# Optimization experiments

Hardware: AMD Instinct MI355X
Metric: run time of the kernel (lower is better)

Reference implementation:

```python
import jax, jax.numpy as jnp
import numpy as np

N, E, F_IN, EDGE_DIM, H, C, NUM_RELS = 20000, 160000, 64, 8, 4, 128, 4


def setup_inputs() -> dict:
    key = jax.random.key(0)
    ks = jax.random.split(key, 20)
    def rn(k, shape, s=0.05):
        return jax.random.normal(k, shape, jnp.float32) * s
    return {
        "x": rn(ks[0], (N, F_IN), 1.0),
        "edge_index": jax.random.randint(ks[1], (2, E), 0, N, dtype=jnp.int32),
        "edge_features": rn(ks[2], (E, EDGE_DIM), 1.0),
        "W1": rn(ks[3], (F_IN, H * C)), "a_src1": rn(ks[4], (H, C)), "a_dst1": rn(ks[5], (H, C)),
        "We1": rn(ks[6], (EDGE_DIM, H * C)), "a_e1": rn(ks[7], (H, C)), "b1": jnp.zeros((H * C,), jnp.float32),
        "W2": rn(ks[8], (H * C, H * C)), "a_src2": rn(ks[9], (H, C)), "a_dst2": rn(ks[10], (H, C)),
        "We2": rn(ks[11], (EDGE_DIM, H * C)), "a_e2": rn(ks[12], (H, C)), "b2": jnp.zeros((H * C,), jnp.float32),
        "Wd1": rn(ks[13], (2 * H * C, 256)), "bd1": jnp.zeros((256,), jnp.float32),
        "Wd2": rn(ks[14], (256, NUM_RELS)), "bd2": jnp.zeros((NUM_RELS,), jnp.float32),
    }


def _add_self_loops(ei, ea, n):
    # PyG add_self_loops with fill_value='mean': self-loop edge_attr is the
    # mean of incoming edge_attr per destination node (0 if no incoming edges).
    dst = ei[1]
    s = jax.ops.segment_sum(ea, dst, num_segments=n)
    cnt = jax.ops.segment_sum(jnp.ones((ea.shape[0], 1), ea.dtype), dst, num_segments=n)
    mean = s / jnp.maximum(cnt, 1.0)
    loop = jnp.arange(n, dtype=ei.dtype)
    ei2 = jnp.concatenate([ei, jnp.stack([loop, loop])], axis=1)
    ea2 = jnp.concatenate([ea, mean], axis=0)
    return ei2, ea2


def _gat_conv(x, ei, ea, W, a_s, a_d, We, a_e, b, n):
    ei, ea = _add_self_loops(ei, ea, n)
    src, dst = ei[0], ei[1]
    xp = (x @ W).reshape(n, H, C)                      # [N,H,C]
    alpha_s = jnp.einsum('nhc,hc->nh', xp, a_s)        # [N,H]
    alpha_d = jnp.einsum('nhc,hc->nh', xp, a_d)        # [N,H]
    ep = (ea @ We).reshape(-1, H, C)                   # [E',H,C]
    alpha_e = jnp.einsum('ehc,hc->eh', ep, a_e)        # [E',H]
    alpha = alpha_s[src] + alpha_d[dst] + alpha_e
    alpha = jax.nn.leaky_relu(alpha, 0.2)
    # segment softmax over edges sharing a destination node
    m = jax.ops.segment_max(alpha, dst, num_segments=n)
    ex = jnp.exp(alpha - m[dst])
    den = jax.ops.segment_sum(ex, dst, num_segments=n)
    w = ex / den[dst]                                   # [E',H]
    out = jax.ops.segment_sum(xp[src] * w[..., None], dst, num_segments=n)  # [N,H,C]
    return out.reshape(n, H * C) + b


def reference(x, edge_index, edge_features, W1, a_src1, a_dst1, We1, a_e1, b1,
              W2, a_src2, a_dst2, We2, a_e2, b2, Wd1, bd1, Wd2, bd2):
    n = x.shape[0]
    z = jax.nn.elu(_gat_conv(x, edge_index, edge_features, W1, a_src1, a_dst1, We1, a_e1, b1, n))
    z = jax.nn.elu(_gat_conv(z, edge_index, edge_features, W2, a_src2, a_dst2, We2, a_e2, b2, n))
    src, dst = edge_index[0], edge_index[1]
    rel = jnp.concatenate([z[src], z[dst]], axis=1)     # [E, 2*512]
    h = rel @ Wd1 + bd1                                 # dropout is identity at inference
    return jax.nn.sigmoid(h @ Wd2 + bd2)
```

## Files before the change

kernel.cpp:

```cpp
#include <hip/hip_runtime.h>
#include <hip/hip_bf16.h>
#include <math.h>

#define N_NODES 20000
#define N_EDGES 160000
#define FIN 64
#define EDGE_DIM 8
#define H_HEADS 4
#define C_CH 128
#define HC 512
#define NUM_RELS 4
#define E_TOT (N_EDGES + N_NODES)
#define E_PAD 320256

typedef __bf16 bf16x8 __attribute__((ext_vector_type(8)));
typedef __bf16 bf16x4 __attribute__((ext_vector_type(4)));
typedef float f32x4 __attribute__((ext_vector_type(4)));
typedef unsigned short u16x8 __attribute__((ext_vector_type(8)));

#define NZ4 ((N_NODES + E_PAD) / 4)
#define NM4 (E_PAD / 4)
__global__ void k_fill(int4* __restrict__ zbase, int4* __restrict__ mbase) {
    int tid = blockIdx.x * 256 + threadIdx.x;
    if (tid < NZ4) {
        zbase[tid] = make_int4(0, 0, 0, 0);
    } else if (tid < NZ4 + NM4) {
        mbase[tid - NZ4] = make_int4(-1, -1, -1, -1);
    }
}

#define NX4 (N_NODES * FIN / 4)
#define XB  (NX4 / 256)
#define W1B 8
#define W2B 64
#define PREPB 19
__global__ void k_prep_all(const float* __restrict__ x, __bf16* __restrict__ xb,
                           const float* __restrict__ W1, __bf16* __restrict__ Wt1,
                           const float* __restrict__ W2, __bf16* __restrict__ Wt2,
                           const float* __restrict__ We1, const float* __restrict__ ae1,
                           const float* __restrict__ We2, const float* __restrict__ ae2,
                           float* __restrict__ q1, float* __restrict__ q2,
                           const float* __restrict__ Wd1, const float* __restrict__ Wd2,
                           const float* __restrict__ bd1, const float* __restrict__ bd2,
                           float* __restrict__ M, float* __restrict__ cvec,
                           const float* __restrict__ as1, const float* __restrict__ ad1,
                           float* __restrict__ w1as, float* __restrict__ w1ad) {
    __shared__ float tile[64][65];
    int bid = blockIdx.x;
    int t = threadIdx.x;
    if (bid < XB) {
        int tid = bid * 256 + t;
        float4 v = *(const float4*)(x + (size_t)tid * 4);
        __bf16 o[4] = {(__bf16)v.x, (__bf16)v.y, (__bf16)v.z, (__bf16)v.w};
        *(ushort2*)(xb + (size_t)tid * 4) = *(ushort2*)o;
        *(ushort2*)(xb + (size_t)tid * 4 + 2) = *(ushort2*)(o + 2);
        return;
    }
    if (bid < XB + W1B) {
        int tn = bid - XB;
        int rr = t >> 6, cc = t & 63;
        #pragma unroll
        for (int i = 0; i < 16; ++i) {
            int row = rr * 16 + i;
            tile[row][cc] = W1[(size_t)row * HC + tn * 64 + cc];
        }
        __syncthreads();
        #pragma unroll
        for (int i = 0; i < 16; ++i) {
            int row = rr * 16 + i;
            Wt1[(size_t)(tn * 64 + row) * 64 + cc] = (__bf16)tile[cc][row];
        }
        return;
    }
    if (bid < XB + W1B + W2B) {
        int p2 = bid - XB - W1B;
        int tk = p2 >> 3, tn = p2 & 7;
        int rr = t >> 6, cc = t & 63;
        #pragma unroll
        for (int i = 0; i < 16; ++i) {
            int row = rr * 16 + i;
            tile[row][cc] = W2[(size_t)(tk * 64 + row) * HC + tn * 64 + cc];
        }
        __syncthreads();
        #pragma unroll
        for (int i = 0; i < 16; ++i) {
            int row = rr * 16 + i;
            Wt2[(size_t)(tn * 64 + row) * HC + tk * 64 + cc] = (__bf16)tile[cc][row];
        }
        return;
    }
    int pb = bid - XB - W1B - W2B;
    if (pb == 16) {
        if (t >= 64) return;
        const float* We = (t < 32) ? We1 : We2;
        const float* ae = (t < 32) ? ae1 : ae2;
        float* q = (t < 32) ? q1 : q2;
        int i = t & 31, h = i >> 3, d = i & 7;
        float s = 0.f;
        for (int c = 0; c < 128; ++c) s += We[d * 512 + h * 128 + c] * ae[h * 128 + c];
        q[i] = s;
    } else if (pb == 17 || pb == 18) {
        int h = t >> 6, k = t & 63;
        const float* av = (pb == 17) ? as1 : ad1;
        float* outp = (pb == 17) ? w1as : w1ad;
        float s = 0.f;
        for (int c = 0; c < 128; ++c) s += W1[(size_t)k * HC + h * 128 + c] * av[h * 128 + c];
        outp[h * 64 + k] = s;
    } else {
        int tid = pb * 256 + t;
        int i = tid >> 2, r = tid & 3;
        float s = 0.f;
        for (int k = 0; k < 256; ++k) s += Wd1[i * 256 + k] * Wd2[k * 4 + r];
        M[tid] = s;
        if (tid < 4) {
            float c = 0.f;
            for (int k = 0; k < 256; ++k) c += bd1[k] * Wd2[k * 4 + tid];
            cvec[tid] = c + bd2[tid];
        }
    }
}

#define LDP 40
__global__ __launch_bounds__(256)
void k_gemm_bf16(const __bf16* __restrict__ A, const __bf16* __restrict__ Bt,
                 __bf16* __restrict__ Ch, int M, int K,
                 const float* __restrict__ a_s2, const float* __restrict__ a_d2,
                 float* __restrict__ as_, float* __restrict__ ad_) {
    __shared__ __bf16 As[128 * LDP];
    __shared__ __bf16 Bs[128 * LDP];

    int nwg = gridDim.x;
    int f = blockIdx.x;
    int q = nwg >> 3, r = nwg & 7;
    int xcd = f & 7, idx = f >> 3;
    int wg = (xcd < r ? xcd * (q + 1) : r * (q + 1) + (xcd - r) * q) + idx;
    int by = wg >> 2, bx = wg & 3;
    int br = by * 128, bc = bx * 128;

    const int t = threadIdx.x;
    const int lane = t & 63;
    const int wid = t >> 6;
    const int wr = wid >> 1, wc = wid & 1;
    const int l15 = lane & 15, lkg = lane >> 4;

    const int srow = t >> 1, shalf = (t & 1) * 16;
    const int agr = br + srow;
    const __bf16* Ap = A + (size_t)agr * K + shalf;
    const __bf16* Bp = Bt + (size_t)(bc + srow) * K + shalf;

    f32x4 acc[4][4] = {};

    for (int k0 = 0; k0 < K; k0 += 32) {
        u16x8 av0 = {}, av1 = {};
        if (agr < M) {
            av0 = *(const u16x8*)(Ap + k0);
            av1 = *(const u16x8*)(Ap + k0 + 8);
        }
        u16x8 bv0 = *(const u16x8*)(Bp + k0);
        u16x8 bv1 = *(const u16x8*)(Bp + k0 + 8);
        *(u16x8*)(As + srow * LDP + shalf) = av0;
        *(u16x8*)(As + srow * LDP + shalf + 8) = av1;
        *(u16x8*)(Bs + srow * LDP + shalf) = bv0;
        *(u16x8*)(Bs + srow * LDP + shalf + 8) = bv1;
        __syncthreads();

        bf16x8 a[4], b[4];
        #pragma unroll
        for (int m = 0; m < 4; ++m)
            a[m] = *(const bf16x8*)(As + (wr * 64 + m * 16 + l15) * LDP + lkg * 8);
        #pragma unroll
        for (int n = 0; n < 4; ++n)
            b[n] = *(const bf16x8*)(Bs + (wc * 64 + n * 16 + l15) * LDP + lkg * 8);
        #pragma unroll
        for (int m = 0; m < 4; ++m)
            #pragma unroll
            for (int n = 0; n < 4; ++n)
                acc[m][n] = __builtin_amdgcn_mfma_f32_16x16x32_bf16(a[m], b[n], acc[m][n], 0, 0, 0);
        __syncthreads();
    }

    #pragma unroll
    for (int m = 0; m < 4; ++m) {
        int rbase = br + wr * 64 + m * 16 + lkg * 4;
        #pragma unroll
        for (int n = 0; n < 4; ++n) {
            int lcol = wc * 64 + n * 16 + l15;
            #pragma unroll
            for (int rg = 0; rg < 4; ++rg) {
                int gr = rbase + rg;
                if (gr < M)
                    Ch[((size_t)bx * N_NODES + gr) * 128 + lcol] = (__bf16)acc[m][n][rg];
            }
        }
    }

    float as_w[4], ad_w[4];
    #pragma unroll
    for (int n = 0; n < 4; ++n) {
        int col = wc * 64 + n * 16 + l15;
        as_w[n] = a_s2[bx * 128 + col];
        ad_w[n] = a_d2[bx * 128 + col];
    }
    float* sred = (float*)As;
    #pragma unroll
    for (int m = 0; m < 4; ++m) {
        #pragma unroll
        for (int rg = 0; rg < 4; ++rg) {
            float s = 0.f, d = 0.f;
            #pragma unroll
            for (int n = 0; n < 4; ++n) {
                float c = acc[m][n][rg];
                s += c * as_w[n];
                d += c * ad_w[n];
            }
            #pragma unroll
            for (int off = 1; off <= 8; off <<= 1) {
                s += __shfl_xor(s, off);
                d += __shfl_xor(d, off);
            }
            if (l15 == 0) {
                int lrow = wr * 64 + m * 16 + lkg * 4 + rg;
                sred[lrow * 2 + wc] = s;
                sred[256 + lrow * 2 + wc] = d;
            }
        }
    }
    __syncthreads();
    if (t < 128) {
        int gr = br + t;
        if (gr < M) {
            as_[gr * 4 + bx] = sred[t * 2] + sred[t * 2 + 1];
            ad_[gr * 4 + bx] = sred[256 + t * 2] + sred[256 + t * 2 + 1];
        }
    }
}

__global__ __launch_bounds__(256)
void k_gemm_head(const __bf16* __restrict__ aggb, const __bf16* __restrict__ Wt1,
                 const float* __restrict__ b1, __bf16* __restrict__ z1b, int M) {
    __shared__ __bf16 As[128 * LDP];
    __shared__ __bf16 Bs[128 * LDP];
    const int h = blockIdx.x;
    const int br = blockIdx.y * 128;

    const int t = threadIdx.x;
    const int lane = t & 63;
    const int wid = t >> 6;
    const int wr = wid >> 1, wc = wid & 1;
    const int l15 = lane & 15, lkg = lane >> 4;

    const int srow = t >> 1, shalf = (t & 1) * 16;
    const int agr = br + srow;
    const __bf16* Ap = aggb + (size_t)agr * 256 + h * 64 + shalf;
    const __bf16* Bp = Wt1 + (size_t)(h * 128 + srow) * 64 + shalf;

    f32x4 acc[4][4] = {};

    #pragma unroll
    for (int k0 = 0; k0 < 64; k0 += 32) {
        u16x8 av0 = {}, av1 = {};
        if (agr < M) {
            av0 = *(const u16x8*)(Ap + k0);
            av1 = *(const u16x8*)(Ap + k0 + 8);
        }
        u16x8 bv0 = *(const u16x8*)(Bp + k0);
        u16x8 bv1 = *(const u16x8*)(Bp + k0 + 8);
        *(u16x8*)(As + srow * LDP + shalf) = av0;
        *(u16x8*)(As + srow * LDP + shalf + 8) = av1;
        *(u16x8*)(Bs + srow * LDP + shalf) = bv0;
        *(u16x8*)(Bs + srow * LDP + shalf + 8) = bv1;
        __syncthreads();

        bf16x8 a[4], b[4];
        #pragma unroll
        for (int m = 0; m < 4; ++m)
            a[m] = *(const bf16x8*)(As + (wr * 64 + m * 16 + l15) * LDP + lkg * 8);
        #pragma unroll
        for (int n = 0; n < 4; ++n)
            b[n] = *(const bf16x8*)(Bs + (wc * 64 + n * 16 + l15) * LDP + lkg * 8);
        #pragma unroll
        for (int m = 0; m < 4; ++m)
            #pragma unroll
            for (int n = 0; n < 4; ++n)
                acc[m][n] = __builtin_amdgcn_mfma_f32_16x16x32_bf16(a[m], b[n], acc[m][n], 0, 0, 0);
        __syncthreads();
    }

    #pragma unroll
    for (int m = 0; m < 4; ++m) {
        int rbase = br + wr * 64 + m * 16 + lkg * 4;
        #pragma unroll
        for (int n = 0; n < 4; ++n) {
            int gcol = h * 128 + wc * 64 + n * 16 + l15;
            float bias = b1[gcol];
            #pragma unroll
            for (int rg = 0; rg < 4; ++rg) {
                int gr = rbase + rg;
                if (gr < M) {
                    float v = acc[m][n][rg] + bias;
                    v = (v > 0.f) ? v : expm1f(v);
                    z1b[(size_t)gr * HC + gcol] = (__bf16)v;
                }
            }
        }
    }
}

__global__ void k_count(const int* __restrict__ ei, int* __restrict__ counts) {
    int e = blockIdx.x * 256 + threadIdx.x;
    if (e >= E_TOT) return;
    int dst = (e < N_EDGES) ? ei[N_EDGES + e] : (e - N_EDGES);
    atomicAdd(counts + dst, 1);
}

__global__ __launch_bounds__(1024)
void k_scan(const int* __restrict__ counts, int* __restrict__ row_start,
            int* __restrict__ nxt) {
    __shared__ int part[1024];
    int t = threadIdx.x;
    int base = t * 20;
    int pre[20];
    int s = 0;
    #pragma unroll
    for (int i = 0; i < 20; ++i) {
        int idx = base + i;
        int c = (idx < N_NODES) ? ((counts[idx] + 7) & ~7) : 0;
        pre[i] = s; s += c;
    }
    part[t] = s;
    __syncthreads();
    for (int off = 1; off < 1024; off <<= 1) {
        int v = (t >= off) ? part[t - off] : 0;
        __syncthreads();
        part[t] += v;
        __syncthreads();
    }
    int excl = (t == 0) ? 0 : part[t - 1];
    #pragma unroll
    for (int i = 0; i < 20; ++i) {
        int idx = base + i;
        if (idx < N_NODES) { int v = excl + pre[i]; row_start[idx] = v; nxt[idx] = v; }
    }
    if (t == 1023) row_start[N_NODES] = part[1023];
}

__global__ void k_scatter(const int* __restrict__ ei, int* __restrict__ nxt,
                          int* __restrict__ csr_src, int* __restrict__ csr_eid,
                          int* __restrict__ csr_dst) {
    int e = blockIdx.x * 256 + threadIdx.x;
    if (e >= E_TOT) return;
    int src, dst;
    if (e < N_EDGES) { src = ei[e]; dst = ei[N_EDGES + e]; }
    else             { src = dst = e - N_EDGES; }
    int pos = atomicAdd(nxt + dst, 1);
    csr_src[pos] = src;
    csr_eid[pos] = e;
    csr_dst[pos] = dst;
}

__global__ void k_mean_csr(const int* __restrict__ row_start, const int* __restrict__ csr_eid,
                           const float* __restrict__ ef, float* __restrict__ meanf) {
    int n = blockIdx.x * 32 + (threadIdx.x >> 3);
    int d = threadIdx.x & 7;
    if (n >= N_NODES) return;
    int rs = row_start[n], re = row_start[n + 1];
    float s = 0.f; int c = 0;
    for (int i = rs; i < re; ++i) {
        unsigned eid = (unsigned)csr_eid[i];
        if (eid < N_EDGES) { s += ef[(size_t)eid * 8 + d]; ++c; }
    }
    meanf[n * 8 + d] = s / fmaxf((float)c, 1.f);
}

__global__ __launch_bounds__(256)
void k_nodeab(const __bf16* __restrict__ xb, const float* __restrict__ w1as,
              const float* __restrict__ w1ad, float* __restrict__ as_,
              float* __restrict__ ad_) {
    int n = blockIdx.x * 4 + (threadIdx.x >> 6);
    int lane = threadIdx.x & 63;
    if (n >= N_NODES) return;
    float xv = (float)xb[(size_t)n * 64 + lane];
    float s[4], d[4];
    #pragma unroll
    for (int h = 0; h < 4; ++h) {
        s[h] = xv * w1as[h * 64 + lane];
        d[h] = xv * w1ad[h * 64 + lane];
    }
    #pragma unroll
    for (int off = 32; off; off >>= 1) {
        #pragma unroll
        for (int h = 0; h < 4; ++h) {
            s[h] += __shfl_xor(s[h], off);
            d[h] += __shfl_xor(d[h], off);
        }
    }
    if (lane == 0) {
        *(float4*)(as_ + n * 4) = make_float4(s[0], s[1], s[2], s[3]);
        *(float4*)(ad_ + n * 4) = make_float4(d[0], d[1], d[2], d[3]);
    }
}

__global__ void k_edge_ex(const int* __restrict__ csr_src, const int* __restrict__ csr_dst,
                          const int* __restrict__ csr_eid, const float* __restrict__ ef,
                          const float* __restrict__ meanf, const float* __restrict__ q,
                          const float* __restrict__ as_, const float* __restrict__ ad_,
                          float* __restrict__ wbuf) {
    int i = blockIdx.x * 256 + threadIdx.x;
    if (i >= E_PAD) return;
    int eid = csr_eid[i];
    if (eid == -1) {
        *(float4*)(wbuf + (size_t)i * 4) = make_float4(0.f, 0.f, 0.f, 0.f);
        return;
    }
    int src = csr_src[i], dst = csr_dst[i];
    const float* fe = (eid < N_EDGES) ? (ef + (size_t)eid * 8)
                                      : (meanf + (size_t)(eid - N_EDGES) * 8);
    float f[8];
    #pragma unroll
    for (int d = 0; d < 8; ++d) f[d] = fe[d];
    float4 asv = *(const float4*)(as_ + src * 4);
    float4 adv = *(const float4*)(ad_ + dst * 4);
    const float* asp = &asv.x;
    const float* adp = &adv.x;
    float4 o;
    float* op = &o.x;
    #pragma unroll
    for (int h = 0; h < 4; ++h) {
        float ae = 0.f;
        #pragma unroll
        for (int d = 0; d < 8; ++d) ae += f[d] * q[h * 8 + d];
        float a = asp[h] + adp[h] + ae;
        a = (a > 0.f) ? a : 0.2f * a;
        op[h] = expf(a);
    }
    *(float4*)(wbuf + (size_t)i * 4) = o;
}

__global__ __launch_bounds__(256)
void k_gather1(const int* __restrict__ row_start, const int* __restrict__ csr_src,
               const float* __restrict__ wbuf, const __bf16* __restrict__ xb,
               __bf16* __restrict__ aggb) {
    int wv = threadIdx.x >> 6;
    int n = blockIdx.x * 4 + wv;
    int lane = threadIdx.x & 63;
    if (n >= N_NODES) return;
    int rs = row_start[n], re = row_start[n + 1];
    float acc[4] = {};
    float den[4] = {};

    for (int i = rs; i < re; i += 8) {
        unsigned short xr[8];
        float4 wr[8];
        #pragma unroll
        for (int p = 0; p < 8; ++p) {
            int sp = csr_src[i + p];
            xr[p] = *(const unsigned short*)(xb + (size_t)sp * 64 + lane);
            wr[p] = *(const float4*)(wbuf + (size_t)(i + p) * 4);
        }
        __builtin_amdgcn_sched_barrier(0);
        #pragma unroll
        for (int p = 0; p < 8; ++p) {
            float xv = (float)*(const __bf16*)&xr[p];
            acc[0] += wr[p].x * xv; den[0] += wr[p].x;
            acc[1] += wr[p].y * xv; den[1] += wr[p].y;
            acc[2] += wr[p].z * xv; den[2] += wr[p].z;
            acc[3] += wr[p].w * xv; den[3] += wr[p].w;
        }
    }
    #pragma unroll
    for (int h = 0; h < 4; ++h)
        aggb[(size_t)n * 256 + h * 64 + lane] = (__bf16)(acc[h] / den[h]);
}

__global__ __launch_bounds__(256)
void k_gather2h(const int* __restrict__ row_start, const int* __restrict__ csr_src,
                const float* __restrict__ wbuf, const __bf16* __restrict__ xph,
                const float* __restrict__ b2, const float* __restrict__ Mm,
                float* __restrict__ Up, float* __restrict__ Vp) {
    int h = blockIdx.y;
    int wv = threadIdx.x >> 6;
    int n = blockIdx.x * 4 + wv;
    int lane = threadIdx.x & 63;
    if (n >= N_NODES) return;
    int rs = row_start[n], re = row_start[n + 1];
    const __bf16* xbase = xph + (size_t)h * N_NODES * 128 + lane * 2;
    float a0 = 0.f, a1 = 0.f, den = 0.f;

    int i = rs;
    for (; i + 16 <= re; i += 16) {
        unsigned xr[16];
        float wr[16];
        #pragma unroll
        for (int p = 0; p < 16; ++p) {
            int sp = csr_src[i + p];
            wr[p] = wbuf[(size_t)(i + p) * 4 + h];
            xr[p] = *(const unsigned*)(xbase + (size_t)sp * 128);
        }
        __builtin_amdgcn_sched_barrier(0);
        #pragma unroll
        for (int p = 0; p < 16; ++p) {
            __bf16 b0 = *(const __bf16*)&xr[p];
            __bf16 b1v = *((const __bf16*)&xr[p] + 1);
            den += wr[p];
            a0 += wr[p] * (float)b0;
            a1 += wr[p] * (float)b1v;
        }
    }
    for (; i < re; i += 8) {
        unsigned xr[8];
        float wr[8];
        #pragma unroll
        for (int p = 0; p < 8; ++p) {
            int sp = csr_src[i + p];
            wr[p] = wbuf[(size_t)(i + p) * 4 + h];
            xr[p] = *(const unsigned*)(xbase + (size_t)sp * 128);
        }
        __builtin_amdgcn_sched_barrier(0);
        #pragma unroll
        for (int p = 0; p < 8; ++p) {
            __bf16 b0 = *(const __bf16*)&xr[p];
            __bf16 b1v = *((const __bf16*)&xr[p] + 1);
            den += wr[p];
            a0 += wr[p] * (float)b0;
            a1 += wr[p] * (float)b1v;
        }
    }
    float inv = 1.f / den;
    float v0 = a0 * inv + b2[h * 128 + lane * 2];
    float v1 = a1 * inv + b2[h * 128 + lane * 2 + 1];
    v0 = (v0 > 0.f) ? v0 : expm1f(v0);
    v1 = (v1 > 0.f) ? v1 : expm1f(v1);

    const float* m0 = Mm + (h * 128 + lane * 2) * 4;
    const float* n0 = Mm + 2048 + (h * 128 + lane * 2) * 4;
    float up[4], vp[4];
    #pragma unroll
    for (int r = 0; r < 4; ++r) {
        up[r] = v0 * m0[r] + v1 * m0[4 + r];
        vp[r] = v0 * n0[r] + v1 * n0[4 + r];
    }
    #pragma unroll
    for (int off = 32; off; off >>= 1) {
        #pragma unroll
        for (int r = 0; r < 4; ++r) {
            up[r] += __shfl_xor(up[r], off);
            vp[r] += __shfl_xor(vp[r], off);
        }
    }
    if (lane == 0) {
        *(float4*)(Up + ((size_t)h * N_NODES + n) * 4) = make_float4(up[0], up[1], up[2], up[3]);
        *(float4*)(Vp + ((size_t)h * N_NODES + n) * 4) = make_float4(vp[0], vp[1], vp[2], vp[3]);
    }
}

__global__ void k_edge_out(const int* __restrict__ ei, const float* __restrict__ Up,
                           const float* __restrict__ Vp, const float* __restrict__ cvec,
                           float* __restrict__ out) {
    int e = blockIdx.x * 256 + threadIdx.x;
    if (e >= N_EDGES) return;
    int s = ei[e], d = ei[N_EDGES + e];
    float4 u = make_float4(0.f, 0.f, 0.f, 0.f);
    float4 v = make_float4(0.f, 0.f, 0.f, 0.f);
    #pragma unroll
    for (int h = 0; h < 4; ++h) {
        float4 uh = *(const float4*)(Up + ((size_t)h * N_NODES + s) * 4);
        float4 vh = *(const float4*)(Vp + ((size_t)h * N_NODES + d) * 4);
        u.x += uh.x; u.y += uh.y; u.z += uh.z; u.w += uh.w;
        v.x += vh.x; v.y += vh.y; v.z += vh.z; v.w += vh.w;
    }
    float4 c = *(const float4*)cvec;
    float4 o;
    o.x = 1.f / (1.f + expf(-(u.x + v.x + c.x)));
    o.y = 1.f / (1.f + expf(-(u.y + v.y + c.y)));
    o.z = 1.f / (1.f + expf(-(u.z + v.z + c.z)));
    o.w = 1.f / (1.f + expf(-(u.w + v.w + c.w)));
    *(float4*)(out + (size_t)e * 4) = o;
}

extern "C" void kernel_launch(void* const* d_in, const int* in_sizes, int n_in,
                              void* d_out, int out_size, void* d_ws, size_t ws_size,
                              hipStream_t stream) {
    (void)in_sizes; (void)n_in; (void)out_size; (void)ws_size;
    const float* x      = (const float*)d_in[0];
    const int*   ei     = (const int*)d_in[1];
    const float* ef     = (const float*)d_in[2];
    const float* W1     = (const float*)d_in[3];
    const float* a_src1 = (const float*)d_in[4];
    const float* a_dst1 = (const float*)d_in[5];
    const float* We1    = (const float*)d_in[6];
    const float* a_e1   = (const float*)d_in[7];
    const float* b1     = (const float*)d_in[8];
    const float* W2     = (const float*)d_in[9];
    const float* a_src2 = (const float*)d_in[10];
    const float* a_dst2 = (const float*)d_in[11];
    const float* We2    = (const float*)d_in[12];
    const float* a_e2   = (const float*)d_in[13];
    const float* b2     = (const float*)d_in[14];
    const float* Wd1    = (const float*)d_in[15];
    const float* bd1    = (const float*)d_in[16];
    const float* Wd2    = (const float*)d_in[17];
    const float* bd2    = (const float*)d_in[18];
    float* out = (float*)d_out;

    float* wbuf   = (float*)d_ws;
    float* as_    = wbuf + (size_t)E_PAD * 4;
    float* ad_    = as_ + N_NODES * 4;
    float* meanf  = ad_ + N_NODES * 4;
    float* q1     = meanf + N_NODES * 8;
    float* q2     = q1 + 32;
    float* w1as   = q2 + 32;
    float* w1ad   = w1as + 256;
    float* Mm     = w1ad + 256;
    float* cv     = Mm + 4096;
    float* Up     = cv + 4;
    float* Vp     = Up + (size_t)N_NODES * 16;
    int* row_start = (int*)(Vp + (size_t)N_NODES * 16);
    int* nxt       = row_start + 20004;
    int* counts    = nxt + N_NODES;
    int* csr_src   = counts + N_NODES;
    int* csr_eid   = csr_src + E_PAD;
    int* csr_dst   = csr_eid + E_PAD;
    __bf16* xb   = (__bf16*)(csr_dst + E_PAD);
    __bf16* aggb = xb + (size_t)N_NODES * FIN;
    __bf16* z1b  = aggb + (size_t)N_NODES * 256;
    __bf16* xph2 = z1b + (size_t)N_NODES * HC;
    __bf16* Wt1  = xph2 + (size_t)N_NODES * HC;
    __bf16* Wt2  = Wt1 + HC * FIN;

    k_fill<<<(NZ4 + NM4 + 255) / 256, 256, 0, stream>>>((int4*)counts, (int4*)csr_eid);
    k_count<<<(E_TOT + 255) / 256, 256, 0, stream>>>(ei, counts);
    k_scan<<<1, 1024, 0, stream>>>(counts, row_start, nxt);
    k_scatter<<<(E_TOT + 255) / 256, 256, 0, stream>>>(ei, nxt, csr_src, csr_eid, csr_dst);
    k_mean_csr<<<(N_NODES + 31) / 32, 256, 0, stream>>>(row_start, csr_eid, ef, meanf);
    k_prep_all<<<XB + W1B + W2B + PREPB, 256, 0, stream>>>(x, xb, W1, Wt1, W2, Wt2,
                                                           We1, a_e1, We2, a_e2, q1, q2,
                                                           Wd1, Wd2, bd1, bd2, Mm, cv,
                                                           a_src1, a_dst1, w1as, w1ad);

    const int nblk = (N_NODES + 3) / 4;
    const int nby = (N_NODES + 127) / 128;

    k_nodeab<<<nblk, 256, 0, stream>>>(xb, w1as, w1ad, as_, ad_);
    k_edge_ex<<<(E_PAD + 255) / 256, 256, 0, stream>>>(csr_src, csr_dst, csr_eid, ef, meanf,
                                                       q1, as_, ad_, wbuf);
    k_gather1<<<nblk, 256, 0, stream>>>(row_start, csr_src, wbuf, xb, aggb);
    k_gemm_head<<<dim3(4, nby), 256, 0, stream>>>(aggb, Wt1, b1, z1b, N_NODES);

    k_gemm_bf16<<<nby * 4, 256, 0, stream>>>(z1b, Wt2, xph2, N_NODES, HC,
                                             a_src2, a_dst2, as_, ad_);
    k_edge_ex<<<(E_PAD + 255) / 256, 256, 0, stream>>>(csr_src, csr_dst, csr_eid, ef, meanf,
                                                       q2, as_, ad_, wbuf);
    k_gather2h<<<dim3(nblk, 4), 256, 0, stream>>>(row_start, csr_src, wbuf, xph2, b2,
                                                  Mm, Up, Vp);

    k_edge_out<<<(N_EDGES + 255) / 256, 256, 0, stream>>>(ei, Up, Vp, cv, out);
}
```

Baseline: 230.8 us.

## Compute edge weights in original edge order and scatter to CSR slots

k_edge_ex now walks edges in their original order. It reads src/dst and edge features with coalesced loads, then writes the exp weights to the CSR slot recorded by k_scatter, so csr_dst is no longer needed. The padding slots of wbuf are now zeroed once by the k_fill kernel instead of per layer, and the workspace is reordered so that one contiguous fill covers them. The gather kernels also use readfirstlane on the row bounds to keep them scalar. The trade is scattered writes to wbuf in place of gathered reads of features and node attributes.

```diff
diff --git a/kernel.cpp b/kernel.cpp
--- a/kernel.cpp
+++ b/kernel.cpp
@@ -18,7 +18,7 @@
 typedef float f32x4 __attribute__((ext_vector_type(4)));
 typedef unsigned short u16x8 __attribute__((ext_vector_type(8)));
 
-#define NZ4 ((N_NODES + E_PAD) / 4)
+#define NZ4 ((5 * E_PAD + N_NODES) / 4)
 #define NM4 (E_PAD / 4)
 __global__ void k_fill(int4* __restrict__ zbase, int4* __restrict__ mbase) {
     int tid = blockIdx.x * 256 + threadIdx.x;
@@ -346,7 +346,7 @@
 
 __global__ void k_scatter(const int* __restrict__ ei, int* __restrict__ nxt,
                           int* __restrict__ csr_src, int* __restrict__ csr_eid,
-                          int* __restrict__ csr_dst) {
+                          int* __restrict__ slot_of_e) {
     int e = blockIdx.x * 256 + threadIdx.x;
     if (e >= E_TOT) return;
     int src, dst;
@@ -355,7 +355,7 @@
     int pos = atomicAdd(nxt + dst, 1);
     csr_src[pos] = src;
     csr_eid[pos] = e;
-    csr_dst[pos] = dst;
+    slot_of_e[e] = pos;
 }
 
 __global__ void k_mean_csr(const int* __restrict__ row_start, const int* __restrict__ csr_eid,
@@ -400,21 +400,16 @@
     }
 }
 
-__global__ void k_edge_ex(const int* __restrict__ csr_src, const int* __restrict__ csr_dst,
-                          const int* __restrict__ csr_eid, const float* __restrict__ ef,
-                          const float* __restrict__ meanf, const float* __restrict__ q,
-                          const float* __restrict__ as_, const float* __restrict__ ad_,
-                          float* __restrict__ wbuf) {
-    int i = blockIdx.x * 256 + threadIdx.x;
-    if (i >= E_PAD) return;
-    int eid = csr_eid[i];
-    if (eid == -1) {
-        *(float4*)(wbuf + (size_t)i * 4) = make_float4(0.f, 0.f, 0.f, 0.f);
-        return;
-    }
-    int src = csr_src[i], dst = csr_dst[i];
-    const float* fe = (eid < N_EDGES) ? (ef + (size_t)eid * 8)
-                                      : (meanf + (size_t)(eid - N_EDGES) * 8);
+__global__ void k_edge_ex(const int* __restrict__ ei, const int* __restrict__ slot_of_e,
+                          const float* __restrict__ ef, const float* __restrict__ meanf,
+                          const float* __restrict__ q, const float* __restrict__ as_,
+                          const float* __restrict__ ad_, float* __restrict__ wbuf) {
+    int e = blockIdx.x * 256 + threadIdx.x;
+    if (e >= E_TOT) return;
+    int src, dst;
+    const float* fe;
+    if (e < N_EDGES) { src = ei[e]; dst = ei[N_EDGES + e]; fe = ef + (size_t)e * 8; }
+    else             { src = dst = e - N_EDGES; fe = meanf + (size_t)(e - N_EDGES) * 8; }
     float f[8];
     #pragma unroll
     for (int d = 0; d < 8; ++d) f[d] = fe[d];
@@ -433,7 +428,7 @@
         a = (a > 0.f) ? a : 0.2f * a;
         op[h] = expf(a);
     }
-    *(float4*)(wbuf + (size_t)i * 4) = o;
+    *(float4*)(wbuf + (size_t)slot_of_e[e] * 4) = o;
 }
 
 __global__ __launch_bounds__(256)
@@ -444,7 +439,8 @@
     int n = blockIdx.x * 4 + wv;
     int lane = threadIdx.x & 63;
     if (n >= N_NODES) return;
-    int rs = row_start[n], re = row_start[n + 1];
+    int rs = __builtin_amdgcn_readfirstlane(row_start[n]);
+    int re = __builtin_amdgcn_readfirstlane(row_start[n + 1]);
     float acc[4] = {};
     float den[4] = {};
 
@@ -482,7 +478,8 @@
     int n = blockIdx.x * 4 + wv;
     int lane = threadIdx.x & 63;
     if (n >= N_NODES) return;
-    int rs = row_start[n], re = row_start[n + 1];
+    int rs = __builtin_amdgcn_readfirstlane(row_start[n]);
+    int re = __builtin_amdgcn_readfirstlane(row_start[n + 1]);
     const __bf16* xbase = xph + (size_t)h * N_NODES * 128 + lane * 2;
     float a0 = 0.f, a1 = 0.f, den = 0.f;
 
@@ -602,8 +599,14 @@
     const float* bd2    = (const float*)d_in[18];
     float* out = (float*)d_out;
 
-    float* wbuf   = (float*)d_ws;
-    float* as_    = wbuf + (size_t)E_PAD * 4;
+    float* wbuf    = (float*)d_ws;
+    int* counts    = (int*)(wbuf + (size_t)E_PAD * 4);
+    int* csr_src   = counts + N_NODES;
+    int* csr_eid   = csr_src + E_PAD;
+    int* slot_of_e = csr_eid + E_PAD;
+    int* row_start = slot_of_e + E_TOT;
+    int* nxt       = row_start + 20004;
+    float* as_    = (float*)(nxt + N_NODES);
     float* ad_    = as_ + N_NODES * 4;
     float* meanf  = ad_ + N_NODES * 4;
     float* q1     = meanf + N_NODES * 8;
@@ -614,23 +617,17 @@
     float* cv     = Mm + 4096;
     float* Up     = cv + 4;
     float* Vp     = Up + (size_t)N_NODES * 16;
-    int* row_start = (int*)(Vp + (size_t)N_NODES * 16);
-    int* nxt       = row_start + 20004;
-    int* counts    = nxt + N_NODES;
-    int* csr_src   = counts + N_NODES;
-    int* csr_eid   = csr_src + E_PAD;
-    int* csr_dst   = csr_eid + E_PAD;
-    __bf16* xb   = (__bf16*)(csr_dst + E_PAD);
+    __bf16* xb   = (__bf16*)(Vp + (size_t)N_NODES * 16);
     __bf16* aggb = xb + (size_t)N_NODES * FIN;
     __bf16* z1b  = aggb + (size_t)N_NODES * 256;
     __bf16* xph2 = z1b + (size_t)N_NODES * HC;
     __bf16* Wt1  = xph2 + (size_t)N_NODES * HC;
     __bf16* Wt2  = Wt1 + HC * FIN;
 
-    k_fill<<<(NZ4 + NM4 + 255) / 256, 256, 0, stream>>>((int4*)counts, (int4*)csr_eid);
+    k_fill<<<(NZ4 + NM4 + 255) / 256, 256, 0, stream>>>((int4*)wbuf, (int4*)csr_eid);
     k_count<<<(E_TOT + 255) / 256, 256, 0, stream>>>(ei, counts);
     k_scan<<<1, 1024, 0, stream>>>(counts, row_start, nxt);
-    k_scatter<<<(E_TOT + 255) / 256, 256, 0, stream>>>(ei, nxt, csr_src, csr_eid, csr_dst);
+    k_scatter<<<(E_TOT + 255) / 256, 256, 0, stream>>>(ei, nxt, csr_src, csr_eid, slot_of_e);
     k_mean_csr<<<(N_NODES + 31) / 32, 256, 0, stream>>>(row_start, csr_eid, ef, meanf);
     k_prep_all<<<XB + W1B + W2B + PREPB, 256, 0, stream>>>(x, xb, W1, Wt1, W2, Wt2,
                                                            We1, a_e1, We2, a_e2, q1, q2,
@@ -641,14 +638,14 @@
     const int nby = (N_NODES + 127) / 128;
 
     k_nodeab<<<nblk, 256, 0, stream>>>(xb, w1as, w1ad, as_, ad_);
-    k_edge_ex<<<(E_PAD + 255) / 256, 256, 0, stream>>>(csr_src, csr_dst, csr_eid, ef, meanf,
+    k_edge_ex<<<(E_TOT + 255) / 256, 256, 0, stream>>>(ei, slot_of_e, ef, meanf,
                                                        q1, as_, ad_, wbuf);
     k_gather1<<<nblk, 256, 0, stream>>>(row_start, csr_src, wbuf, xb, aggb);
     k_gemm_head<<<dim3(4, nby), 256, 0, stream>>>(aggb, Wt1, b1, z1b, N_NODES);
 
     k_gemm_bf16<<<nby * 4, 256, 0, stream>>>(z1b, Wt2, xph2, N_NODES, HC,
                                              a_src2, a_dst2, as_, ad_);
-    k_edge_ex<<<(E_PAD + 255) / 256, 256, 0, stream>>>(csr_src, csr_dst, csr_eid, ef, meanf,
+    k_edge_ex<<<(E_TOT + 255) / 256, 256, 0, stream>>>(ei, slot_of_e, ef, meanf,
                                                        q2, as_, ad_, wbuf);
     k_gather2h<<<dim3(nblk, 4), 256, 0, stream>>>(row_start, csr_src, wbuf, xph2, b2,
                                                   Mm, Up, Vp);
```

Measured after the change: 224.9 us. -2.6%, faster.
